# Kernel optimization log

Hardware: AMD Instinct MI355X
Metric: run time of the kernel (lower is better)

## Reference

```python
import jax, jax.numpy as jnp
import numpy as np
import math

B, NQ, D = 2, 5000, 256
HEADS, LVLS, PTS, NREF = 8, 4, 8, 4  # PTS = all_sampling_points, NREF = ref points per query
DH = D // HEADS
SHAPES = [(100, 100), (50, 50), (25, 25), (13, 13)]
NV = sum(h * w for h, w in SHAPES)


def _grid_init_bias():
    # replicates DeformableSatAttention.init_weights sampling_offsets bias
    thetas = np.arange(HEADS, dtype=np.float32) * (2.0 * math.pi / HEADS)
    grid = np.stack([np.cos(thetas), np.sin(thetas)], -1)
    grid = grid / np.abs(grid).max(-1, keepdims=True)
    grid = np.tile(grid.reshape(HEADS, 1, 1, 2), (1, LVLS, PTS, 1))  # PTS == HEADS
    for i in range(PTS):
        grid[:, :, i, :] *= i + 1
    return jnp.asarray(grid.reshape(-1), dtype=jnp.float32)


def setup_inputs() -> dict:
    key = jax.random.key(0)
    ks = jax.random.split(key, 8)
    xb = math.sqrt(6.0 / (D + D))  # xavier uniform bound for value_proj
    return {
        "query": jax.random.normal(ks[0], (B, NQ, D), jnp.float32),
        "key": jax.random.normal(ks[1], (B, NV, D), jnp.float32),
        "value": jax.random.normal(ks[2], (B, NV, D), jnp.float32),
        "reference_points": jax.random.uniform(ks[3], (B, NQ, NREF, 2), jnp.float32),
        "spatial_shapes": jnp.asarray(SHAPES, jnp.int32),
        "level_start_index": jnp.asarray(np.cumsum([0] + [h * w for h, w in SHAPES])[:-1], jnp.int32),
        "W_value": jax.random.uniform(ks[4], (D, D), jnp.float32, -xb, xb),
        "b_value": jnp.zeros((D,), jnp.float32),
        "W_offset": 0.01 * jax.random.normal(ks[5], (D, HEADS * LVLS * PTS * 2), jnp.float32),
        "b_offset": _grid_init_bias(),
        "W_attn": 0.01 * jax.random.normal(ks[6], (D, HEADS * LVLS * PTS), jnp.float32),
        "b_attn": jnp.zeros((HEADS * LVLS * PTS,), jnp.float32),
    }


def _bilinear(vflat, H, W, loc):
    # vflat: [B, H*W, HEADS, DH]; loc: [B, NQ, HEADS, PTS, 2] in [0,1]
    # grid_sample-style align_corners=False, zero padding (as in MSDeformAttn CUDA)
    x = loc[..., 0] * W - 0.5
    y = loc[..., 1] * H - 0.5
    x0 = jnp.floor(x)
    y0 = jnp.floor(y)
    dx = x - x0
    dy = y - y0
    x0i = x0.astype(jnp.int32)
    y0i = y0.astype(jnp.int32)

    def gather(ix, iy):
        valid = ((ix >= 0) & (ix < W) & (iy >= 0) & (iy < H)).astype(vflat.dtype)
        idx = jnp.clip(iy, 0, H - 1) * W + jnp.clip(ix, 0, W - 1)  # [B,NQ,HEADS,PTS]
        b, nq, h, p = idx.shape
        idx2 = idx.transpose(0, 1, 3, 2).reshape(b, nq * p, h)
        g = jnp.take_along_axis(vflat, idx2[..., None], axis=1)  # [B,NQ*PTS,HEADS,DH]
        g = g.reshape(b, nq, p, h, -1).transpose(0, 1, 3, 2, 4)  # [B,NQ,HEADS,PTS,DH]
        return g * valid[..., None]

    g00 = gather(x0i, y0i)
    g01 = gather(x0i + 1, y0i)
    g10 = gather(x0i, y0i + 1)
    g11 = gather(x0i + 1, y0i + 1)
    w00 = ((1 - dx) * (1 - dy))[..., None]
    w01 = (dx * (1 - dy))[..., None]
    w10 = ((1 - dx) * dy)[..., None]
    w11 = (dx * dy)[..., None]
    return g00 * w00 + g01 * w01 + g10 * w10 + g11 * w11


def reference(query, key, value, reference_points, spatial_shapes, level_start_index,
              W_value, b_value, W_offset, b_offset, W_attn, b_attn):
    bs, nq, _ = query.shape
    v = (value @ W_value + b_value).reshape(bs, -1, HEADS, DH)
    off = (query @ W_offset + b_offset).reshape(bs, nq, HEADS, LVLS, PTS, 2)
    aw = jax.nn.softmax((query @ W_attn + b_attn).reshape(bs, nq, HEADS, LVLS * PTS), axis=-1)
    aw = aw.reshape(bs, nq, HEADS, LVLS, PTS)
    shapes = np.asarray(spatial_shapes)  # static level geometry
    starts = np.asarray(level_start_index)
    # offset_normalizer = (W, H) per level
    norm = jnp.asarray(np.stack([shapes[:, 1], shapes[:, 0]], -1), jnp.float32)
    off = off / norm[None, None, None, :, None, :]
    off = off.reshape(bs, nq, HEADS, LVLS, PTS // NREF, NREF, 2)
    loc = reference_points[:, :, None, None, None, :, :] + off
    loc = loc.reshape(bs, nq, HEADS, LVLS, PTS, 2)
    out = jnp.zeros((bs, nq, HEADS, DH), v.dtype)
    for l in range(shapes.shape[0]):
        Hl, Wl = int(shapes[l, 0]), int(shapes[l, 1])
        s = int(starts[l])
        vl = v[:, s:s + Hl * Wl]
        sampled = _bilinear(vl, Hl, Wl, loc[:, :, :, l])  # [B,NQ,HEADS,PTS,DH]
        out = out + (sampled * aw[:, :, :, l][..., None]).sum(axis=3)
    return out.reshape(bs, nq, D)
```

## Files before the change

### kernel.cpp

```cpp
#include <hip/hip_runtime.h>
#include <math.h>

#define HEADS 8
#define LVLS  4
#define PTS   8
#define NREF  4
#define DH    32
#define DD    256
#define NQc   5000
#define BATCH 2
#define NVc   13294
#define RVr   (BATCH * NVc)
#define RQr   (BATCH * NQc)

#define NJV 832
#define NJQ 942
#define NJOBS (NJV + NJQ)

#define NEV (RVr * 256)
#define NEQ (RQr * 256)
#define NCV ((NEV + 4095) / 4096)
#define NCQ ((NEQ + 4095) / 4096)

using f16x8 = __attribute__((ext_vector_type(8))) _Float16;
using f16x4 = __attribute__((ext_vector_type(4))) _Float16;
using f32x4 = __attribute__((ext_vector_type(4))) float;
using h2    = __attribute__((ext_vector_type(2))) _Float16;

__device__ __forceinline__ int pack2(float w) {
    _Float16 h = (_Float16)w;
    h2 v = { h, h };
    return __builtin_bit_cast(int, v);
}

__global__ __launch_bounds__(256) void prep_kernel(
    const float* __restrict__ value, const float* __restrict__ query,
    const float* __restrict__ Wv, const float* __restrict__ Wo,
    const float* __restrict__ Wa,
    _Float16* __restrict__ a16v, _Float16* __restrict__ a16q,
    _Float16* __restrict__ wtv, _Float16* __restrict__ wto,
    _Float16* __restrict__ wta)
{
    const int bid = blockIdx.x;
    const int t   = threadIdx.x;
    if (bid < 64) {
        __shared__ float tl[64][65];
        const float* src; _Float16* dst; int N, kt, nt;
        if (bid < 16)      { src = Wv; dst = wtv; N = 256; kt = bid & 3;        nt = bid >> 2; }
        else if (bid < 48) { src = Wo; dst = wto; N = 512; kt = (bid - 16) & 3; nt = (bid - 16) >> 2; }
        else               { src = Wa; dst = wta; N = 256; kt = (bid - 48) & 3; nt = (bid - 48) >> 2; }
        const int k0 = kt * 64, n0 = nt * 64;
        const int c  = t & 63, r4 = t >> 6;
        #pragma unroll
        for (int i = 0; i < 16; ++i) {
            const int r = r4 + i * 4;
            tl[r][c] = src[(size_t)(k0 + r) * N + n0 + c];
        }
        __syncthreads();
        #pragma unroll
        for (int i = 0; i < 16; ++i) {
            const int r = r4 + i * 4;
            dst[(size_t)(n0 + r) * 256 + k0 + c] = (_Float16)tl[c][r];
        }
        return;
    }
    const int cid = bid - 64;
    const float* src; _Float16* dst; int n; size_t base;
    if (cid < NCV) { src = value; dst = a16v; n = NEV; base = (size_t)cid * 4096; }
    else           { src = query; dst = a16q; n = NEQ; base = (size_t)(cid - NCV) * 4096; }
    #pragma unroll
    for (int i = 0; i < 4; ++i) {
        const size_t idx = base + i * 1024 + t * 4;
        if (idx < (size_t)n) {
            const float4 v = *(const float4*)&src[idx];
            f16x4 pk = { (_Float16)v.x, (_Float16)v.y, (_Float16)v.z, (_Float16)v.w };
            *(f16x4*)&dst[idx] = pk;
        }
    }
}

__global__ __launch_bounds__(256) void gemm_uber_kernel(
    const _Float16* __restrict__ a16v, const _Float16* __restrict__ a16q,
    const _Float16* __restrict__ wtv, const _Float16* __restrict__ wtoa,
    const float* __restrict__ bv, const float* __restrict__ bo,
    const float* __restrict__ ba,
    _Float16* __restrict__ v_f16, _Float16* __restrict__ offa)
{
    __shared__ _Float16 aL[64][64];
    __shared__ _Float16 bL[128][64];

    const int t    = threadIdx.x;
    const int lane = t & 63;
    const int wid  = t >> 6;
    const int wr   = wid >> 1;
    const int wc   = wid & 1;

    const int job = blockIdx.x;
    const bool isV = job < NJV;
    const _Float16* A; const _Float16* WT; int r0, ct;
    if (isV) { A = a16v; WT = wtv;  r0 = (job >> 1) * 64;  ct = job & 1; }
    else     { const int j2 = job - NJV;
               A = a16q; WT = wtoa; r0 = (j2 / 6) * 64;    ct = j2 % 6; }
    const int c0 = ct * 128;

    f32x4 acc[2][4] = {};

    const int brow  = lane >> 3;
    const int bslot = (lane & 7) ^ brow;
    const int lm  = lane & 15;
    const int khi = lane >> 4;

    for (int kc = 0; kc < 256; kc += 64) {
        __syncthreads();
        #pragma unroll
        for (int cch = 0; cch < 4; ++cch) {
            const int ch  = wid * 4 + cch;
            const int row = ch * 8 + brow;
            const _Float16* src = WT + (size_t)(c0 + row) * 256 + kc + bslot * 8;
            char* ldst = (char*)&bL[0][0] + ch * 1024;
            __builtin_amdgcn_global_load_lds(
                (const __attribute__((address_space(1))) void*)src,
                (__attribute__((address_space(3))) void*)ldst, 16, 0, 0);
        }
        #pragma unroll
        for (int cch = 0; cch < 2; ++cch) {
            const int ch  = wid * 2 + cch;
            const int row = ch * 8 + brow;
            const _Float16* src = A + (size_t)(r0 + row) * 256 + kc + bslot * 8;
            char* ldst = (char*)&aL[0][0] + ch * 1024;
            __builtin_amdgcn_global_load_lds(
                (const __attribute__((address_space(1))) void*)src,
                (__attribute__((address_space(3))) void*)ldst, 16, 0, 0);
        }
        __syncthreads();

        const char* bB = (const char*)&bL[0][0];
        const char* aB = (const char*)&aL[0][0];
        #pragma unroll
        for (int kk = 0; kk < 2; ++kk) {
            const int slot = kk * 4 + khi;
            f16x8 bfrag[4];
            #pragma unroll
            for (int nf = 0; nf < 4; ++nf) {
                const int row = wc * 64 + nf * 16 + lm;
                bfrag[nf] = *(const f16x8*)(bB + row * 128 + ((slot ^ (row & 7)) << 4));
            }
            #pragma unroll
            for (int m = 0; m < 2; ++m) {
                const int arow = wr * 32 + m * 16 + lm;
                const f16x8 afrag = *(const f16x8*)(aB + arow * 128 + ((slot ^ (arow & 7)) << 4));
                #pragma unroll
                for (int nf = 0; nf < 4; ++nf)
                    acc[m][nf] = __builtin_amdgcn_mfma_f32_16x16x32_f16(
                        afrag, bfrag[nf], acc[m][nf], 0, 0, 0);
            }
        }
    }

    const int lq = lane >> 4;
    if (isV) {
        #pragma unroll
        for (int nf = 0; nf < 4; ++nf) {
            const int col = c0 + wc * 64 + nf * 16 + lm;
            const int hh = col >> 5, ch = col & 31;
            const float bb = bv[col];
            #pragma unroll
            for (int m = 0; m < 2; ++m)
                #pragma unroll
                for (int r = 0; r < 4; ++r) {
                    const int row = r0 + wr * 32 + m * 16 + lq * 4 + r;
                    if (row < RVr) {
                        const int b   = (row >= NVc) ? 1 : 0;
                        const int pix = row - b * NVc;
                        v_f16[(((size_t)(b * HEADS + hh) * NVc) + pix) * 32 + ch] =
                            (_Float16)(acc[m][nf][r] + bb);
                    }
                }
        }
    } else {
        #pragma unroll
        for (int nf = 0; nf < 4; ++nf) {
            const int col = c0 + wc * 64 + nf * 16 + lm;
            const float bb = (col < 512) ? bo[col] : ba[col - 512];
            #pragma unroll
            for (int m = 0; m < 2; ++m)
                #pragma unroll
                for (int r = 0; r < 4; ++r) {
                    const int row = r0 + wr * 32 + m * 16 + lq * 4 + r;
                    if (row < RQr) offa[(size_t)row * 768 + col] = (_Float16)(acc[m][nf][r] + bb);
                }
        }
    }
}

__global__ __launch_bounds__(256) void sample_kernel(
    const _Float16* __restrict__ v,
    const _Float16* __restrict__ offa,
    const float* __restrict__ refp,
    float* __restrict__ out)
{
    __shared__ int2 swa[4][32][5];

    const int t    = threadIdx.x;
    const int wv   = t >> 6;
    const int lane = t & 63;
    const int j    = lane & 31;
    const int half = lane >> 5;

    const int task = blockIdx.x * 4 + wv;
    const int h  = task & 7;
    const int bq = task >> 3;
    const int b  = bq / NQc;

    {
        const int l = j >> 3;
        const int p = j & 7;
        const int r = p & 3;
        const int   Wi = (l == 0) ? 100 : (l == 1) ? 50 : (l == 2) ? 25 : 13;
        const float Wf = (float)Wi;
        const int   st = (l == 0) ? 0 : (l == 1) ? 10000 : (l == 2) ? 12500 : 13125;

        const _Float16* orow = offa + (size_t)bq * 768;
        const float lg = (float)orow[512 + h * 32 + j];
        const float e  = __expf(lg);
        float s = e;
        #pragma unroll
        for (int mask = 16; mask >= 1; mask >>= 1)
            s += __shfl_xor(s, mask, 64);
        const float aw = __fdividef(e, s);

        const h2 oxy = *(const h2*)&orow[h * 64 + j * 2];
        const float2 rxy = *(const float2*)&refp[((size_t)bq * NREF + r) * 2];

        const float x = rxy.x * Wf + (float)oxy[0] - 0.5f;
        const float y = rxy.y * Wf + (float)oxy[1] - 0.5f;
        const float x0f = floorf(x), y0f = floorf(y);
        const float dx = x - x0f, dy = y - y0f;
        const int x0 = (int)x0f, y0 = (int)y0f;
        const int x1 = x0 + 1;

        const int   yy = y0 + half;
        const float fy = (half ? dy : 1.f - dy) * aw;
        const bool  vy = (yy >= 0) && (yy < Wi);
        const int   yc = min(max(yy, 0), Wi - 1);

        const bool vx0 = (x0 >= 0) && (x0 < Wi);
        const bool vx1 = (x1 >= 0) && (x1 < Wi);
        const int  xc0 = min(max(x0, 0), Wi - 1);
        const int  xc1 = min(max(x1, 0), Wi - 1);

        const int bb   = ((b * HEADS + h) * NVc + st) * 64;
        const int rowb = bb + yc * Wi * 64;
        const float wA = (vx0 && vy) ? (1.f - dx) * fy : 0.f;
        const float wB = (vx1 && vy) ? dx * fy : 0.f;

        swa[wv][j][half * 2 + 0] = make_int2(rowb + (xc0 << 6), pack2(wA));
        swa[wv][j][half * 2 + 1] = make_int2(rowb + (xc1 << 6), pack2(wB));
    }

    const int po  = lane >> 4;
    const int c   = (lane >> 2) & 3;
    const int cqb = (lane & 3) * 16;

    int2 aw8[8];
    #pragma unroll
    for (int it = 0; it < 8; ++it)
        aw8[it] = swa[wv][it * 4 + po][c];

    f16x8 val[8];
    #pragma unroll
    for (int it = 0; it < 8; ++it)
        val[it] = *(const f16x8*)((const char*)v + aw8[it].x + cqb);

    h2 acc0 = {}, acc1 = {}, acc2 = {}, acc3 = {};
    #pragma unroll
    for (int it = 0; it < 8; ++it) {
        const h2 w2 = __builtin_bit_cast(h2, aw8[it].y);
        acc0 += w2 * (h2){ val[it][0], val[it][1] };
        acc1 += w2 * (h2){ val[it][2], val[it][3] };
        acc2 += w2 * (h2){ val[it][4], val[it][5] };
        acc3 += w2 * (h2){ val[it][6], val[it][7] };
    }

    #pragma unroll
    for (int mask = 4; mask <= 32; mask <<= 1) {
        acc0 += __builtin_bit_cast(h2, __shfl_xor(__builtin_bit_cast(int, acc0), mask, 64));
        acc1 += __builtin_bit_cast(h2, __shfl_xor(__builtin_bit_cast(int, acc1), mask, 64));
        acc2 += __builtin_bit_cast(h2, __shfl_xor(__builtin_bit_cast(int, acc2), mask, 64));
        acc3 += __builtin_bit_cast(h2, __shfl_xor(__builtin_bit_cast(int, acc3), mask, 64));
    }

    if (lane < 4) {
        float* dst = &out[(size_t)bq * 256 + h * 32 + lane * 8];
        *(float4*)(dst + 0) = make_float4((float)acc0[0], (float)acc0[1],
                                          (float)acc1[0], (float)acc1[1]);
        *(float4*)(dst + 4) = make_float4((float)acc2[0], (float)acc2[1],
                                          (float)acc3[0], (float)acc3[1]);
    }
}

extern "C" void kernel_launch(void* const* d_in, const int* in_sizes, int n_in,
                              void* d_out, int out_size, void* d_ws, size_t ws_size,
                              hipStream_t stream)
{
    const float* query  = (const float*)d_in[0];
    const float* value  = (const float*)d_in[2];
    const float* refp   = (const float*)d_in[3];
    const float* Wv     = (const float*)d_in[6];
    const float* bv     = (const float*)d_in[7];
    const float* Wo     = (const float*)d_in[8];
    const float* bo     = (const float*)d_in[9];
    const float* Wa     = (const float*)d_in[10];
    const float* ba     = (const float*)d_in[11];
    float* out = (float*)d_out;

    _Float16* a16v  = (_Float16*)d_ws;
    _Float16* a16q  = a16v + (size_t)RVr * 256;
    _Float16* v_f16 = a16q + (size_t)RQr * 256;
    _Float16* offa  = v_f16 + (size_t)RVr * 256;
    _Float16* wtv   = offa + (size_t)RQr * 768;
    _Float16* wtoa  = wtv + 256 * 256;

    prep_kernel<<<dim3(64 + NCV + NCQ), 256, 0, stream>>>(
        value, query, Wv, Wo, Wa, a16v, a16q, wtv, wtoa, wtoa + 512 * 256);

    gemm_uber_kernel<<<dim3(NJOBS), 256, 0, stream>>>(
        a16v, a16q, wtv, wtoa, bv, bo, ba, v_f16, offa);

    sample_kernel<<<dim3(RQr * HEADS / 4), 256, 0, stream>>>(
        v_f16, offa, refp, out);
}
```

Baseline: 76.56 us.

## Remap deformable sampling to one block per query with 32 threads per head

The sampling kernel now gives each block one query, with all 8 heads handled by 32-thread groups, instead of one wavefront per (query, head) task. Each thread computes all four bilinear corners for its sampling point. Each thread then runs a 16-step gather loop instead of issuing 8 fully preloaded loads, and the cross-lane reduction shrinks to within 32 lanes. The goal is fewer blocks and less redundant per-point work. The cost is half as many threads doing the same number of gathers, so each thread has more serial load latency to cover.

```diff
diff --git a/kernel.cpp b/kernel.cpp
--- a/kernel.cpp
+++ b/kernel.cpp
@@ -199,17 +199,12 @@
     const float* __restrict__ refp,
     float* __restrict__ out)
 {
-    __shared__ int2 swa[4][32][5];
-
-    const int t    = threadIdx.x;
-    const int wv   = t >> 6;
-    const int lane = t & 63;
-    const int j    = lane & 31;
-    const int half = lane >> 5;
-
-    const int task = blockIdx.x * 4 + wv;
-    const int h  = task & 7;
-    const int bq = task >> 3;
+    __shared__ int2 swa[8][32][5];
+
+    const int t  = threadIdx.x;
+    const int h  = t >> 5;
+    const int j  = t & 31;
+    const int bq = blockIdx.x;
     const int b  = bq / NQc;
 
     {
@@ -237,61 +232,61 @@
         const float x0f = floorf(x), y0f = floorf(y);
         const float dx = x - x0f, dy = y - y0f;
         const int x0 = (int)x0f, y0 = (int)y0f;
-        const int x1 = x0 + 1;
-
-        const int   yy = y0 + half;
-        const float fy = (half ? dy : 1.f - dy) * aw;
-        const bool  vy = (yy >= 0) && (yy < Wi);
-        const int   yc = min(max(yy, 0), Wi - 1);
+        const int x1 = x0 + 1,  y1 = y0 + 1;
 
         const bool vx0 = (x0 >= 0) && (x0 < Wi);
         const bool vx1 = (x1 >= 0) && (x1 < Wi);
+        const bool vy0 = (y0 >= 0) && (y0 < Wi);
+        const bool vy1 = (y1 >= 0) && (y1 < Wi);
         const int  xc0 = min(max(x0, 0), Wi - 1);
         const int  xc1 = min(max(x1, 0), Wi - 1);
-
-        const int bb   = ((b * HEADS + h) * NVc + st) * 64;
-        const int rowb = bb + yc * Wi * 64;
-        const float wA = (vx0 && vy) ? (1.f - dx) * fy : 0.f;
-        const float wB = (vx1 && vy) ? dx * fy : 0.f;
-
-        swa[wv][j][half * 2 + 0] = make_int2(rowb + (xc0 << 6), pack2(wA));
-        swa[wv][j][half * 2 + 1] = make_int2(rowb + (xc1 << 6), pack2(wB));
-    }
-
-    const int po  = lane >> 4;
-    const int c   = (lane >> 2) & 3;
-    const int cqb = (lane & 3) * 16;
-
-    int2 aw8[8];
+        const int  yc0 = min(max(y0, 0), Wi - 1);
+        const int  yc1 = min(max(y1, 0), Wi - 1);
+
+        const float fy0 = (1.f - dy) * aw;
+        const float fy1 = dy * aw;
+
+        const int bb    = ((b * HEADS + h) * NVc + st) * 64;
+        const int rowb0 = bb + yc0 * Wi * 64;
+        const int rowb1 = bb + yc1 * Wi * 64;
+
+        swa[h][j][0] = make_int2(rowb0 + (xc0 << 6),
+                                 pack2((vx0 && vy0) ? (1.f - dx) * fy0 : 0.f));
+        swa[h][j][1] = make_int2(rowb0 + (xc1 << 6),
+                                 pack2((vx1 && vy0) ? dx * fy0 : 0.f));
+        swa[h][j][2] = make_int2(rowb1 + (xc0 << 6),
+                                 pack2((vx0 && vy1) ? (1.f - dx) * fy1 : 0.f));
+        swa[h][j][3] = make_int2(rowb1 + (xc1 << 6),
+                                 pack2((vx1 && vy1) ? dx * fy1 : 0.f));
+    }
+
+    const int corner = (t >> 3) & 3;
+    const int po     = (t >> 2) & 1;
+    const int cqb    = (t & 3) * 16;
+
+    h2 acc0 = {}, acc1 = {}, acc2 = {}, acc3 = {};
+    #pragma unroll 8
+    for (int it = 0; it < 16; ++it) {
+        const int pp = it * 2 + po;
+        const int2 d = swa[h][pp][corner];
+        const h2 w2 = __builtin_bit_cast(h2, d.y);
+        const f16x8 val = *(const f16x8*)((const char*)v + d.x + cqb);
+        acc0 += w2 * (h2){ val[0], val[1] };
+        acc1 += w2 * (h2){ val[2], val[3] };
+        acc2 += w2 * (h2){ val[4], val[5] };
+        acc3 += w2 * (h2){ val[6], val[7] };
+    }
+
     #pragma unroll
-    for (int it = 0; it < 8; ++it)
-        aw8[it] = swa[wv][it * 4 + po][c];
-
-    f16x8 val[8];
-    #pragma unroll
-    for (int it = 0; it < 8; ++it)
-        val[it] = *(const f16x8*)((const char*)v + aw8[it].x + cqb);
-
-    h2 acc0 = {}, acc1 = {}, acc2 = {}, acc3 = {};
-    #pragma unroll
-    for (int it = 0; it < 8; ++it) {
-        const h2 w2 = __builtin_bit_cast(h2, aw8[it].y);
-        acc0 += w2 * (h2){ val[it][0], val[it][1] };
-        acc1 += w2 * (h2){ val[it][2], val[it][3] };
-        acc2 += w2 * (h2){ val[it][4], val[it][5] };
-        acc3 += w2 * (h2){ val[it][6], val[it][7] };
-    }
-
-    #pragma unroll
-    for (int mask = 4; mask <= 32; mask <<= 1) {
+    for (int mask = 4; mask <= 16; mask <<= 1) {
         acc0 += __builtin_bit_cast(h2, __shfl_xor(__builtin_bit_cast(int, acc0), mask, 64));
         acc1 += __builtin_bit_cast(h2, __shfl_xor(__builtin_bit_cast(int, acc1), mask, 64));
         acc2 += __builtin_bit_cast(h2, __shfl_xor(__builtin_bit_cast(int, acc2), mask, 64));
         acc3 += __builtin_bit_cast(h2, __shfl_xor(__builtin_bit_cast(int, acc3), mask, 64));
     }
 
-    if (lane < 4) {
-        float* dst = &out[(size_t)bq * 256 + h * 32 + lane * 8];
+    if ((t & 0x1c) == 0) {
+        float* dst = &out[(size_t)bq * 256 + h * 32 + (t & 3) * 8];
         *(float4*)(dst + 0) = make_float4((float)acc0[0], (float)acc0[1],
                                           (float)acc1[0], (float)acc1[1]);
         *(float4*)(dst + 4) = make_float4((float)acc2[0], (float)acc2[1],
@@ -327,6 +322,6 @@
     gemm_uber_kernel<<<dim3(NJOBS), 256, 0, stream>>>(
         a16v, a16q, wtv, wtoa, bv, bo, ba, v_f16, offa);
 
-    sample_kernel<<<dim3(RQr * HEADS / 4), 256, 0, stream>>>(
+    sample_kernel<<<dim3(RQr), 256, 0, stream>>>(
         v_f16, offa, refp, out);
 }
```

Result: no change. 77.91 us (+1.8%).
